# Kernel optimization log

Measured on AMD Instinct MI355X. Metric: run time of the kernel, lower is better.

The kernel has to match this reference:

```python
import jax, jax.numpy as jnp
import numpy as np
from jax import lax

STRIDES = (8, 16, 32, 64, 128)
LEVEL_HW = ((100, 128), (50, 64), (25, 32), (13, 16), (7, 8))
NUM_CLASSES = 80
PRE_NMS_THRESH = 0.05
PRE_NMS_TOPK = 1000
NMS_THRESH = 0.6
MAX_DET = 100
CLS_OFFSET = 1.0e4  # > max image coordinate, separates classes for joint NMS


def setup_inputs() -> dict:
    key = jax.random.key(0)
    B = 16
    ks = jax.random.split(key, 3 * len(LEVEL_HW))
    inp = {}
    i = 0
    for lvl, (h, w) in enumerate(LEVEL_HW):
        # shift logits down so sigmoid scores are mostly below the 0.05 candidate
        # threshold (realistic detection sparsity)
        inp[f"logits_p{lvl + 3}"] = jax.random.normal(ks[i], (B, NUM_CLASSES, h, w), jnp.float32) - 4.0; i += 1
        inp[f"bbox_p{lvl + 3}"] = jax.random.uniform(ks[i], (B, 4, h, w), jnp.float32, minval=0.0, maxval=64.0); i += 1
        inp[f"ctr_p{lvl + 3}"] = jax.random.normal(ks[i], (B, 1, h, w), jnp.float32); i += 1
    inp["im_info"] = jnp.tile(jnp.array([[800.0, 1024.0]], jnp.float32), (B, 1))
    return inp


def _locations(h, w, stride):
    # FCOSLocation: center of each stride cell -> [HW, 2] as (x, y)
    sx = jnp.arange(w, dtype=jnp.float32) * stride + stride // 2
    sy = jnp.arange(h, dtype=jnp.float32) * stride + stride // 2
    yy, xx = jnp.meshgrid(sy, sx, indexing="ij")
    return jnp.stack([xx.reshape(-1), yy.reshape(-1)], axis=-1)


def _nms_single(boxes, scores, classes):
    # boxes [K,4], scores [K] (descending), classes [K] int
    off = classes.astype(jnp.float32)[:, None] * CLS_OFFSET
    nb = boxes + off  # class-offset trick -> per-class NMS in one pass
    areas = jnp.maximum(nb[:, 2] - nb[:, 0], 0.0) * jnp.maximum(nb[:, 3] - nb[:, 1], 0.0)

    def body(sc, _):
        i = jnp.argmax(sc)
        s = sc[i]
        bi = nb[i]
        xx1 = jnp.maximum(bi[0], nb[:, 0])
        yy1 = jnp.maximum(bi[1], nb[:, 1])
        xx2 = jnp.minimum(bi[2], nb[:, 2])
        yy2 = jnp.minimum(bi[3], nb[:, 3])
        inter = jnp.maximum(xx2 - xx1, 0.0) * jnp.maximum(yy2 - yy1, 0.0)
        iou = inter / (areas[i] + areas - inter + 1e-9)
        sc2 = jnp.where(iou >= NMS_THRESH, -jnp.inf, sc).at[i].set(-jnp.inf)
        return sc2, (i, s > 0.0)

    _, (idxs, valid) = lax.scan(body, scores, None, length=MAX_DET)
    det = jnp.concatenate(
        [boxes[idxs], scores[idxs][:, None], classes[idxs].astype(jnp.float32)[:, None]],
        axis=-1,
    )  # [MAX_DET, 6] = x1,y1,x2,y2,score,class
    return jnp.where(valid[:, None], det, 0.0)


def _forward(logits_p3, bbox_p3, ctr_p3, logits_p4, bbox_p4, ctr_p4,
             logits_p5, bbox_p5, ctr_p5, logits_p6, bbox_p6, ctr_p6,
             logits_p7, bbox_p7, ctr_p7, im_info):
    levels = [(logits_p3, bbox_p3, ctr_p3), (logits_p4, bbox_p4, ctr_p4),
              (logits_p5, bbox_p5, ctr_p5), (logits_p6, bbox_p6, ctr_p6),
              (logits_p7, bbox_p7, ctr_p7)]
    scores_l, boxes_l = [], []
    for (lg, rg, ct), stride in zip(levels, STRIDES):
        B, C, H, W = lg.shape
        cls = jax.nn.sigmoid(lg).transpose(0, 2, 3, 1).reshape(B, H * W, C)
        cen = jax.nn.sigmoid(ct).transpose(0, 2, 3, 1).reshape(B, H * W, 1)
        # candidate threshold on raw class prob, then modulate by centerness
        comb = jnp.where(cls > PRE_NMS_THRESH, cls * cen, 0.0)
        locs = _locations(H, W, stride)  # [HW, 2]
        reg = rg.transpose(0, 2, 3, 1).reshape(B, H * W, 4)  # (l, t, r, b)
        bx = jnp.stack([locs[None, :, 0] - reg[..., 0],
                        locs[None, :, 1] - reg[..., 1],
                        locs[None, :, 0] + reg[..., 2],
                        locs[None, :, 1] + reg[..., 3]], axis=-1)
        scores_l.append(comb)
        boxes_l.append(bx)
    scores = jnp.concatenate(scores_l, axis=1)  # [B, N, C]
    boxes = jnp.concatenate(boxes_l, axis=1)    # [B, N, 4]
    B, N, C = scores.shape
    vals, idx = lax.top_k(scores.reshape(B, N * C), PRE_NMS_TOPK)  # [B, K]
    loc = idx // C
    cls_id = idx % C
    cand = jnp.take_along_axis(boxes, loc[..., None], axis=1)  # [B, K, 4]
    h = im_info[:, 0:1]
    w = im_info[:, 1:2]
    x1 = jnp.clip(cand[..., 0], 0.0, w - 1.0)
    y1 = jnp.clip(cand[..., 1], 0.0, h - 1.0)
    x2 = jnp.clip(cand[..., 2], 0.0, w - 1.0)
    y2 = jnp.clip(cand[..., 3], 0.0, h - 1.0)
    cand = jnp.stack([x1, y1, x2, y2], axis=-1)
    sc = jnp.where(vals > 0.0, jnp.sqrt(jnp.maximum(vals, 0.0) + 1e-12), 0.0)
    return jax.vmap(_nms_single)(cand, sc, cls_id)  # [B, MAX_DET, 6]


def reference(logits_p3, bbox_p3, ctr_p3, logits_p4, bbox_p4, ctr_p4,
              logits_p5, bbox_p5, ctr_p5, logits_p6, bbox_p6, ctr_p6,
              logits_p7, bbox_p7, ctr_p7, im_info):
    return _forward(logits_p3, bbox_p3, ctr_p3, logits_p4, bbox_p4, ctr_p4,
                    logits_p5, bbox_p5, ctr_p5, logits_p6, bbox_p6, ctr_p6,
                    logits_p7, bbox_p7, ctr_p7, im_info)
```

## Files before the change

kernel.cpp:

```cpp
#include <hip/hip_runtime.h>
#include <math.h>

#pragma clang fp contract(off)

#define NB 16
#define NC 80
#define NTOT 17064
#define TOPK 1000
#define NBINS 8192
#define CAP 4096
#define MAXDET 100
#define CNTSTRIDE 64
#define CHUNK 128
#define GH 128

struct Ptrs {
    const float* lg[5];
    const float* bb[5];
    const float* ct[5];
};

__device__ __forceinline__ void level_of(int n, int& l, int& hw, int& W,
                                         int& stride, int& half, int& HW) {
    if (n < 12800)      { l = 0; hw = n;         W = 128; stride = 8;   half = 4;  HW = 12800; }
    else if (n < 16000) { l = 1; hw = n - 12800; W = 64;  stride = 16;  half = 8;  HW = 3200;  }
    else if (n < 16800) { l = 2; hw = n - 16000; W = 32;  stride = 32;  half = 16; HW = 800;   }
    else if (n < 17008) { l = 3; hw = n - 16800; W = 16;  stride = 64;  half = 32; HW = 208;   }
    else                { l = 4; hw = n - 17008; W = 8;   stride = 128; half = 64; HW = 56;    }
}

__device__ __forceinline__ float fast_sig(float x) {
    float e = __expf(-x);
    return __builtin_amdgcn_rcpf(1.0f + e);
}

#define HG_ELEM(X, CT)                                                        \
    if ((X) > -2.47f) {                             \
        float cls = fast_sig(X);                                              \
        float cen = fast_sig(CT);                                             \
        unsigned bits = __float_as_uint(cls * cen);                           \
        if (bits >= FB_LO) {                                                  \
            int lb = (int)((bits - 32u) >> 19) - BINBASE;                     \
            lb = (lb < 0) ? 0 : ((lb > 63) ? 63 : lb);                        \
            atomicAdd(&whv[lb], 1u);                                          \
        }                                                                     \
    }

template<int HW4, int NF4>
__device__ __forceinline__ void histg_level(const float* lgb, const float* ctb,
        int tid, int bx, int gx, unsigned FB_LO, int BINBASE, unsigned* whv) {
    for (int i0 = bx * 512; i0 < NF4; i0 += gx * 512) {
        int ia = i0 + tid, ib = i0 + 256 + tid;
        bool la = ia < NF4, lb2 = ib < NF4;
        float4 va = make_float4(-9.f, -9.f, -9.f, -9.f);
        float4 vb = make_float4(-9.f, -9.f, -9.f, -9.f);
        int hwa = 0, hwb = 0;
        if (la) {
            int c = ia / HW4; hwa = ia - c * HW4;
            va = *(const float4*)(lgb + c * (HW4 * 4) + hwa * 4);
        }
        if (lb2) {
            int c = ib / HW4; hwb = ib - c * HW4;
            vb = *(const float4*)(lgb + c * (HW4 * 4) + hwb * 4);
        }
        if (va.x > -2.47f || va.y > -2.47f || va.z > -2.47f || va.w > -2.47f) {
            float4 cv = *(const float4*)(ctb + hwa * 4);
            HG_ELEM(va.x, cv.x) HG_ELEM(va.y, cv.y)
            HG_ELEM(va.z, cv.z) HG_ELEM(va.w, cv.w)
        }
        if (vb.x > -2.47f || vb.y > -2.47f || vb.z > -2.47f || vb.w > -2.47f) {
            float4 cv = *(const float4*)(ctb + hwb * 4);
            HG_ELEM(vb.x, cv.x) HG_ELEM(vb.y, cv.y)
            HG_ELEM(vb.z, cv.z) HG_ELEM(vb.w, cv.w)
        }
    }
}
#undef HG_ELEM

__global__ void __launch_bounds__(256) k_histB(Ptrs p, unsigned* hist, unsigned* cnt2) {
    __shared__ unsigned wh[4][64];
    int b = blockIdx.y, tid = threadIdx.x, bx = blockIdx.x, gx = gridDim.x;
    int wv = tid >> 6;
    if (bx == 0 && tid == 0) cnt2[(size_t)b * CNTSTRIDE] = 0;
    ((unsigned*)wh)[tid] = 0;
    __syncthreads();
    unsigned FB_LO = __float_as_uint(0.08f) - 64u;
    int BINBASE = (int)(__float_as_uint(0.08f) >> 19);
    unsigned* whv = wh[wv];

    histg_level<3200, 256000>(p.lg[0] + (size_t)b * NC * 12800, p.ct[0] + (size_t)b * 12800, tid, bx, gx, FB_LO, BINBASE, whv);
    histg_level< 800,  64000>(p.lg[1] + (size_t)b * NC * 3200,  p.ct[1] + (size_t)b * 3200,  tid, bx, gx, FB_LO, BINBASE, whv);
    histg_level< 200,  16000>(p.lg[2] + (size_t)b * NC * 800,   p.ct[2] + (size_t)b * 800,   tid, bx, gx, FB_LO, BINBASE, whv);
    histg_level<  52,   4160>(p.lg[3] + (size_t)b * NC * 208,   p.ct[3] + (size_t)b * 208,   tid, bx, gx, FB_LO, BINBASE, whv);
    histg_level<  14,   1120>(p.lg[4] + (size_t)b * NC * 56,    p.ct[4] + (size_t)b * 56,    tid, bx, gx, FB_LO, BINBASE, whv);

    __syncthreads();
    if (tid < 64) {
        unsigned s = wh[0][tid] + wh[1][tid] + wh[2][tid] + wh[3][tid];
        hist[((size_t)b * GH + bx) * 64 + tid] = s;
    }
}

template<int HW4, int NF4>
__device__ __forceinline__ void histf_level(const float* lgb, const float* ctb,
                                            int tid, unsigned* hist) {
    for (int i0 = 0; i0 < NF4; i0 += 256) {
        int i = i0 + tid;
        if (i < NF4) {
            int c = i / HW4, hwf = i - c * HW4;
            float4 v = *(const float4*)(lgb + c * (HW4 * 4) + hwf * 4);
            if (v.x > -2.95f || v.y > -2.95f || v.z > -2.95f || v.w > -2.95f) {
                float4 cv = *(const float4*)(ctb + hwf * 4);
                float xs[4] = {v.x, v.y, v.z, v.w};
                float cs[4] = {cv.x, cv.y, cv.z, cv.w};
#pragma unroll
                for (int j = 0; j < 4; ++j) {
                    float x = xs[j];
                    if (x > -2.95f) {
                        float cls = fast_sig(x);
                        if (cls > 0.04999f) {
                            bool in = true;
                            if (cls < 0.05001f)
                                in = (1.0f / (1.0f + expf(-x))) > 0.05f;
                            if (in) {
                                float cen = fast_sig(cs[j]);
                                unsigned bits = __float_as_uint(cls * cen);
                                unsigned cb = (bits > 32u) ? bits - 32u : 0u;
                                atomicAdd(&hist[cb >> 19], 1u);
                            }
                        }
                    }
                }
            }
        }
    }
}

__global__ void __launch_bounds__(256) k_thresh(Ptrs p, const unsigned* hist,
                                                unsigned* T) {
    __shared__ unsigned part[4][64];
    __shared__ unsigned red[64];
    __shared__ unsigned fullh[NBINS];
    __shared__ int s_T, s_ok;
    int b = blockIdx.x, tid = threadIdx.x;
    int bin = tid & 63, grp = tid >> 6;
    int BINBASE = (int)(__float_as_uint(0.08f) >> 19);

    unsigned s = 0;
    for (int blk = grp; blk < GH; blk += 4)
        s += hist[((size_t)b * GH + blk) * 64 + bin];
    part[grp][bin] = s;
    __syncthreads();
    if (tid < 64) red[tid] = part[0][tid] + part[1][tid] + part[2][tid] + part[3][tid];
    __syncthreads();
    if (tid == 0) {
        unsigned suf1 = 0;
        for (int i = 1; i < 64; ++i) suf1 += red[i];
        unsigned run = 0; int Tl = 0;
        for (int i = 63; i >= 1; --i) {
            run += red[i];
            if (run >= TOPK) { Tl = i; break; }
        }
        s_ok = (suf1 >= TOPK);
        s_T = Tl + BINBASE;
    }
    __syncthreads();

    if (!s_ok) {
        for (int i = tid; i < NBINS; i += 256) fullh[i] = 0;
        __syncthreads();
        histf_level<3200, 256000>(p.lg[0] + (size_t)b * NC * 12800, p.ct[0] + (size_t)b * 12800, tid, fullh);
        histf_level< 800,  64000>(p.lg[1] + (size_t)b * NC * 3200,  p.ct[1] + (size_t)b * 3200,  tid, fullh);
        histf_level< 200,  16000>(p.lg[2] + (size_t)b * NC * 800,   p.ct[2] + (size_t)b * 800,   tid, fullh);
        histf_level<  52,   4160>(p.lg[3] + (size_t)b * NC * 208,   p.ct[3] + (size_t)b * 208,   tid, fullh);
        histf_level<  14,   1120>(p.lg[4] + (size_t)b * NC * 56,    p.ct[4] + (size_t)b * 56,    tid, fullh);
        __syncthreads();
        if (tid == 0) {
            unsigned run = 0; int Tf = 0;
            for (int i = NBINS - 1; i >= 0; --i) {
                run += fullh[i];
                if (run >= TOPK) { Tf = i; break; }
            }
            s_T = Tf;
        }
        __syncthreads();
    }
    if (tid == 0) T[b] = (unsigned)s_T;
}

#define CD_J(J, X, CT, NB0, CC, F, K)                                         \
    if ((X) > xpre) {                                                         \
        float cls = 1.0f / (1.0f + expf(-(X)));                               \
        if (cls > 0.05f) {                                                    \
            float cen = 1.0f / (1.0f + expf(-(CT)));                          \
            float comb = cls * cen;                                           \
            unsigned bits = __float_as_uint(comb);                            \
            if ((bits >> 19) >= Tb) {                                         \
                unsigned idx = (unsigned)(((NB0) + (J)) * NC + (CC));         \
                K = ((unsigned long long)bits << 32) | (0xFFFFFFFFu - idx);   \
                F = true;                                                     \
            }                                                                 \
        }                                                                     \
    }

template<int HW4, int NF4, int LVOFF>
__device__ __forceinline__ void compact_level(const float* lgb, const float* ctb,
        int tid, int lane, int bx, int gx, unsigned Tb, float xpre,
        unsigned* cntb, unsigned long long* selb, unsigned long long ltmask) {
    for (int i0 = bx * 512; i0 < NF4; i0 += gx * 512) {
        int ia = i0 + tid, ib2 = i0 + 256 + tid;
        bool la = ia < NF4, lb2 = ib2 < NF4;
        float4 va = make_float4(-9.f, -9.f, -9.f, -9.f);
        float4 vb = make_float4(-9.f, -9.f, -9.f, -9.f);
        int hwa = 0, hwb = 0, cca = 0, ccb = 0;
        if (la) {
            cca = ia / HW4; hwa = ia - cca * HW4;
            va = *(const float4*)(lgb + cca * (HW4 * 4) + hwa * 4);
        }
        if (lb2) {
            ccb = ib2 / HW4; hwb = ib2 - ccb * HW4;
            vb = *(const float4*)(lgb + ccb * (HW4 * 4) + hwb * 4);
        }
        {
            bool f0 = false, f1 = false, f2 = false, f3 = false;
            unsigned long long k0 = 0, k1 = 0, k2 = 0, k3 = 0;
            if (va.x > xpre || va.y > xpre || va.z > xpre || va.w > xpre) {
                float4 cv = *(const float4*)(ctb + hwa * 4);
                int nb0 = LVOFF + hwa * 4;
                CD_J(0, va.x, cv.x, nb0, cca, f0, k0)
                CD_J(1, va.y, cv.y, nb0, cca, f1, k1)
                CD_J(2, va.z, cv.z, nb0, cca, f2, k2)
                CD_J(3, va.w, cv.w, nb0, cca, f3, k3)
            }
            unsigned long long m0 = __ballot(f0), m1 = __ballot(f1);
            unsigned long long m2 = __ballot(f2), m3 = __ballot(f3);
            if (m0 | m1 | m2 | m3) {
                unsigned t0 = (unsigned)__popcll(m0), t1 = (unsigned)__popcll(m1);
                unsigned t2 = (unsigned)__popcll(m2), t3 = (unsigned)__popcll(m3);
                int basep = 0;
                if (lane == 0) basep = (int)atomicAdd(cntb, t0 + t1 + t2 + t3);
                basep = __shfl(basep, 0);
                if (f0) { int pos = basep + (int)__popcll(m0 & ltmask);                       if (pos < CAP) selb[pos] = k0; }
                if (f1) { int pos = basep + (int)t0 + (int)__popcll(m1 & ltmask);             if (pos < CAP) selb[pos] = k1; }
                if (f2) { int pos = basep + (int)(t0 + t1) + (int)__popcll(m2 & ltmask);      if (pos < CAP) selb[pos] = k2; }
                if (f3) { int pos = basep + (int)(t0 + t1 + t2) + (int)__popcll(m3 & ltmask); if (pos < CAP) selb[pos] = k3; }
            }
        }
        {
            bool f0 = false, f1 = false, f2 = false, f3 = false;
            unsigned long long k0 = 0, k1 = 0, k2 = 0, k3 = 0;
            if (vb.x > xpre || vb.y > xpre || vb.z > xpre || vb.w > xpre) {
                float4 cv = *(const float4*)(ctb + hwb * 4);
                int nb0 = LVOFF + hwb * 4;
                CD_J(0, vb.x, cv.x, nb0, ccb, f0, k0)
                CD_J(1, vb.y, cv.y, nb0, ccb, f1, k1)
                CD_J(2, vb.z, cv.z, nb0, ccb, f2, k2)
                CD_J(3, vb.w, cv.w, nb0, ccb, f3, k3)
            }
            unsigned long long m0 = __ballot(f0), m1 = __ballot(f1);
            unsigned long long m2 = __ballot(f2), m3 = __ballot(f3);
            if (m0 | m1 | m2 | m3) {
                unsigned t0 = (unsigned)__popcll(m0), t1 = (unsigned)__popcll(m1);
                unsigned t2 = (unsigned)__popcll(m2), t3 = (unsigned)__popcll(m3);
                int basep = 0;
                if (lane == 0) basep = (int)atomicAdd(cntb, t0 + t1 + t2 + t3);
                basep = __shfl(basep, 0);
                if (f0) { int pos = basep + (int)__popcll(m0 & ltmask);                       if (pos < CAP) selb[pos] = k0; }
                if (f1) { int pos = basep + (int)t0 + (int)__popcll(m1 & ltmask);             if (pos < CAP) selb[pos] = k1; }
                if (f2) { int pos = basep + (int)(t0 + t1) + (int)__popcll(m2 & ltmask);      if (pos < CAP) selb[pos] = k2; }
                if (f3) { int pos = basep + (int)(t0 + t1 + t2) + (int)__popcll(m3 & ltmask); if (pos < CAP) selb[pos] = k3; }
            }
        }
    }
}
#undef CD_J

__global__ void __launch_bounds__(256) k_compactB(Ptrs p, const unsigned* T,
                                                  unsigned* cnt2, unsigned long long* sel) {
    int b = blockIdx.y, tid = threadIdx.x, lane = tid & 63;
    int bx = blockIdx.x, gx = gridDim.x;
    unsigned Tb = T[b];
    float mthr = __uint_as_float(Tb << 19);
    float xpre = -2.95f;
    if (mthr > 1e-37f && mthr < 1.0f) {
        float lm = logf(mthr / (1.0f - mthr)) - 0.01f;
        if (lm > xpre) xpre = lm;
    }
    unsigned long long ltmask = (1ULL << lane) - 1ULL;
    unsigned* cntb = cnt2 + (size_t)b * CNTSTRIDE;
    unsigned long long* selb = sel + (size_t)b * CAP;
    compact_level<3200, 256000,     0>(p.lg[0] + (size_t)b * NC * 12800, p.ct[0] + (size_t)b * 12800, tid, lane, bx, gx, Tb, xpre, cntb, selb, ltmask);
    compact_level< 800,  64000, 12800>(p.lg[1] + (size_t)b * NC * 3200,  p.ct[1] + (size_t)b * 3200,  tid, lane, bx, gx, Tb, xpre, cntb, selb, ltmask);
    compact_level< 200,  16000, 16000>(p.lg[2] + (size_t)b * NC * 800,   p.ct[2] + (size_t)b * 800,   tid, lane, bx, gx, Tb, xpre, cntb, selb, ltmask);
    compact_level<  52,   4160, 16800>(p.lg[3] + (size_t)b * NC * 208,   p.ct[3] + (size_t)b * 208,   tid, lane, bx, gx, Tb, xpre, cntb, selb, ltmask);
    compact_level<  14,   1120, 17008>(p.lg[4] + (size_t)b * NC * 56,    p.ct[4] + (size_t)b * 56,    tid, lane, bx, gx, Tb, xpre, cntb, selb, ltmask);
}

__global__ void __launch_bounds__(256) k_rankdec(Ptrs p, const unsigned* cnt,
                                                 const unsigned long long* sel,
                                                 const float* im_info, float* cand) {
    __shared__ __align__(16) unsigned long long keys[CAP];
    int b = blockIdx.y, tid = threadIdx.x;
    unsigned M = cnt[(size_t)b * CNTSTRIDE];
    if (M > CAP) M = CAP;
    int s0 = blockIdx.x * 256;
    if (s0 >= (int)M) return;
    int Mpad = (int)((M + 1u) & ~1u);
    for (int i = tid; i < Mpad; i += 256)
        keys[i] = (i < (int)M) ? sel[(size_t)b * CAP + i] : 0ULL;
    __syncthreads();

    int s = s0 + tid;
    if (s >= (int)M) return;
    unsigned long long k = keys[s];
    int rank = 0;
    for (int j = 0; j < Mpad; j += 2) {
        ulonglong2 kk = *(const ulonglong2*)&keys[j];
        rank += (kk.x > k) ? 1 : 0;
        rank += (kk.y > k) ? 1 : 0;
    }
    if (rank >= TOPK) return;

    float Him = im_info[b * 2 + 0], Wim = im_info[b * 2 + 1];
    float xmax = Wim - 1.0f, ymax = Him - 1.0f;
    unsigned sb = (unsigned)(k >> 32);
    unsigned idx = 0xFFFFFFFFu - (unsigned)(k & 0xFFFFFFFFu);
    float val = __uint_as_float(sb);
    int n = idx / NC, c = idx - n * NC;
    int l, hw, W, stride, half, HW;
    level_of(n, l, hw, W, stride, half, HW);
    int wx = hw % W, hy = hw / W;
    float locx = (float)(wx * stride + half);
    float locy = (float)(hy * stride + half);
    const float* bb = p.bb[l] + (size_t)b * 4 * HW + hw;
    float r0 = bb[0], r1 = bb[(size_t)HW], r2 = bb[(size_t)2 * HW], r3 = bb[(size_t)3 * HW];
    float x1 = locx - r0, y1 = locy - r1, x2 = locx + r2, y2 = locy + r3;
    x1 = fminf(fmaxf(x1, 0.f), xmax);
    y1 = fminf(fmaxf(y1, 0.f), ymax);
    x2 = fminf(fmaxf(x2, 0.f), xmax);
    y2 = fminf(fmaxf(y2, 0.f), ymax);
    float scv = sqrtf(val + 1e-12f);
    float off = (float)c * 10000.0f;
    float a0 = x1 + off, a1 = y1 + off, a2 = x2 + off, a3 = y2 + off;
    float area = fmaxf(a2 - a0, 0.f) * fmaxf(a3 - a1, 0.f);
    float* dst = cand + ((size_t)b * TOPK + rank) * 12;
    *(float4*)(dst + 0) = make_float4(x1, y1, x2, y2);
    *(float4*)(dst + 4) = make_float4(a0, a1, a2, a3);
    *(float4*)(dst + 8) = make_float4(area, scv, (float)c, 0.f);
}

__global__ void __launch_bounds__(64) k_nms(const unsigned* cnt, const float* cand,
                                            float* out) {
    __shared__ float4 s_ob[CHUNK], s_nb[CHUNK], s_ms[CHUNK];
    int b = blockIdx.x, lane = threadIdx.x;
    unsigned M = cnt[(size_t)b * CNTSTRIDE];
    if (M > CAP) M = CAP;
    int ncand = (int)M < TOPK ? (int)M : TOPK;
    const float* src = cand + (size_t)b * TOPK * 12;
    float* ob = out + (size_t)b * MAXDET * 6;

    int na = 0;
    float4 a0b = make_float4(0.f, 0.f, 0.f, 0.f);
    float4 a1b = make_float4(0.f, 0.f, 0.f, 0.f);
    float a0a = 0.f, a1a = 0.f;

    for (int base = 0; base < ncand && na < MAXDET; base += CHUNK) {
        int cn = ncand - base; if (cn > CHUNK) cn = CHUNK;
        for (int cidx = lane; cidx < cn; cidx += 64) {
            const float* s = src + (size_t)(base + cidx) * 12;
            s_ob[cidx] = *(const float4*)(s + 0);
            s_nb[cidx] = *(const float4*)(s + 4);
            s_ms[cidx] = *(const float4*)(s + 8);
        }
        __syncthreads();
        for (int r = 0; r < cn && na < MAXDET; ++r) {
            float4 cb = s_nb[r];
            float ca = s_ms[r].x;
            bool sup = false;
            if (lane < na) {
                float xx1 = fmaxf(a0b.x, cb.x);
                float yy1 = fmaxf(a0b.y, cb.y);
                float xx2 = fminf(a0b.z, cb.z);
                float yy2 = fminf(a0b.w, cb.w);
                float inter = fmaxf(xx2 - xx1, 0.f) * fmaxf(yy2 - yy1, 0.f);
                float iou = inter / (((a0a + ca) - inter) + 1e-9f);
                sup = (iou >= 0.6f);
            }
            if (lane + 64 < na) {
                float xx1 = fmaxf(a1b.x, cb.x);
                float yy1 = fmaxf(a1b.y, cb.y);
                float xx2 = fminf(a1b.z, cb.z);
                float yy2 = fminf(a1b.w, cb.w);
                float inter = fmaxf(xx2 - xx1, 0.f) * fmaxf(yy2 - yy1, 0.f);
                float iou = inter / (((a1a + ca) - inter) + 1e-9f);
                sup |= (iou >= 0.6f);
            }
            if (__ballot(sup) == 0ULL) {
                if (lane == (na & 63)) {
                    if (na < 64) { a0b = cb; a0a = ca; }
                    else         { a1b = cb; a1a = ca; }
                }
                if (lane == 0) {
                    float4 o4 = s_ob[r]; float4 m4 = s_ms[r];
                    ob[na * 6 + 0] = o4.x; ob[na * 6 + 1] = o4.y;
                    ob[na * 6 + 2] = o4.z; ob[na * 6 + 3] = o4.w;
                    ob[na * 6 + 4] = m4.y; ob[na * 6 + 5] = m4.z;
                }
                ++na;
            }
        }
        __syncthreads();
    }
    for (int q = na * 6 + lane; q < MAXDET * 6; q += 64)
        ob[q] = 0.f;
}

extern "C" void kernel_launch(void* const* d_in, const int* in_sizes, int n_in,
                              void* d_out, int out_size, void* d_ws, size_t ws_size,
                              hipStream_t stream) {
    Ptrs p;
    for (int l = 0; l < 5; ++l) {
        p.lg[l] = (const float*)d_in[3 * l + 0];
        p.bb[l] = (const float*)d_in[3 * l + 1];
        p.ct[l] = (const float*)d_in[3 * l + 2];
    }
    const float* im_info = (const float*)d_in[15];
    float* out = (float*)d_out;
    unsigned char* w = (unsigned char*)d_ws;

    unsigned* hist          = (unsigned*)(w);
    unsigned* cnt2          = (unsigned*)(w + 524288);
    unsigned* T             = (unsigned*)(w + 528384);
    unsigned long long* sel = (unsigned long long*)(w + 528640);
    float* cand             = (float*)(w + 1052928);

    k_histB<<<dim3(GH, NB), 256, 0, stream>>>(p, hist, cnt2);
    k_thresh<<<NB, 256, 0, stream>>>(p, hist, T);
    k_compactB<<<dim3(GH, NB), 256, 0, stream>>>(p, T, cnt2, sel);
    k_rankdec<<<dim3(16, NB), 256, 0, stream>>>(p, cnt2, sel, im_info, cand);
    k_nms<<<NB, 64, 0, stream>>>(cnt2, cand, out);
}
```

Before: 237.8 us.

## Record candidate keys during histogram pass and filter them instead of rescanning logits

The histogram kernel now also appends every above-floor candidate (score bits and flat index) to a per-block segment buffer in workspace. A merged threshold+filter kernel then computes the threshold per image and, when no segment overflowed, compacts only those recorded candidates by re-deriving exact scores from gathered logits. This avoids a second full pass over all logits and removes one launch. It falls back to a full rescan on overflow or when the coarse histogram is insufficient, and it adds shared-memory atomics to the hot histogram loop and a larger workspace.

```diff
diff --git a/kernel.cpp b/kernel.cpp
--- a/kernel.cpp
+++ b/kernel.cpp
@@ -13,6 +13,8 @@
 #define CNTSTRIDE 64
 #define CHUNK 128
 #define GH 128
+#define SEGCAP 768
+#define FB 16
 
 struct Ptrs {
     const float* lg[5];
@@ -34,7 +36,7 @@
     return __builtin_amdgcn_rcpf(1.0f + e);
 }
 
-#define HG_ELEM(X, CT)                                                        \
+#define HG_ELEM(X, CT, J, CC, NB0)                                            \
     if ((X) > -2.47f) {                             \
         float cls = fast_sig(X);                                              \
         float cen = fast_sig(CT);                                             \
@@ -43,62 +45,75 @@
             int lb = (int)((bits - 32u) >> 19) - BINBASE;                     \
             lb = (lb < 0) ? 0 : ((lb > 63) ? 63 : lb);                        \
             atomicAdd(&whv[lb], 1u);                                          \
+            unsigned pos = atomicAdd(s_na, 1u);                               \
+            if (pos < SEGCAP) {                                               \
+                unsigned idx = (unsigned)(((NB0) + (J)) * NC + (CC));         \
+                segb[pos] = ((unsigned long long)bits << 32) | idx;           \
+            }                                                                 \
         }                                                                     \
     }
 
-template<int HW4, int NF4>
+template<int HW4, int NF4, int LVOFF>
 __device__ __forceinline__ void histg_level(const float* lgb, const float* ctb,
-        int tid, int bx, int gx, unsigned FB_LO, int BINBASE, unsigned* whv) {
+        int tid, int bx, int gx, unsigned FB_LO, int BINBASE, unsigned* whv,
+        unsigned* s_na, unsigned long long* segb) {
     for (int i0 = bx * 512; i0 < NF4; i0 += gx * 512) {
         int ia = i0 + tid, ib = i0 + 256 + tid;
         bool la = ia < NF4, lb2 = ib < NF4;
         float4 va = make_float4(-9.f, -9.f, -9.f, -9.f);
         float4 vb = make_float4(-9.f, -9.f, -9.f, -9.f);
-        int hwa = 0, hwb = 0;
+        int hwa = 0, hwb = 0, cca = 0, ccb = 0;
         if (la) {
-            int c = ia / HW4; hwa = ia - c * HW4;
-            va = *(const float4*)(lgb + c * (HW4 * 4) + hwa * 4);
+            cca = ia / HW4; hwa = ia - cca * HW4;
+            va = *(const float4*)(lgb + cca * (HW4 * 4) + hwa * 4);
         }
         if (lb2) {
-            int c = ib / HW4; hwb = ib - c * HW4;
-            vb = *(const float4*)(lgb + c * (HW4 * 4) + hwb * 4);
+            ccb = ib / HW4; hwb = ib - ccb * HW4;
+            vb = *(const float4*)(lgb + ccb * (HW4 * 4) + hwb * 4);
         }
         if (va.x > -2.47f || va.y > -2.47f || va.z > -2.47f || va.w > -2.47f) {
             float4 cv = *(const float4*)(ctb + hwa * 4);
-            HG_ELEM(va.x, cv.x) HG_ELEM(va.y, cv.y)
-            HG_ELEM(va.z, cv.z) HG_ELEM(va.w, cv.w)
+            int nb0 = LVOFF + hwa * 4;
+            HG_ELEM(va.x, cv.x, 0, cca, nb0) HG_ELEM(va.y, cv.y, 1, cca, nb0)
+            HG_ELEM(va.z, cv.z, 2, cca, nb0) HG_ELEM(va.w, cv.w, 3, cca, nb0)
         }
         if (vb.x > -2.47f || vb.y > -2.47f || vb.z > -2.47f || vb.w > -2.47f) {
             float4 cv = *(const float4*)(ctb + hwb * 4);
-            HG_ELEM(vb.x, cv.x) HG_ELEM(vb.y, cv.y)
-            HG_ELEM(vb.z, cv.z) HG_ELEM(vb.w, cv.w)
+            int nb0 = LVOFF + hwb * 4;
+            HG_ELEM(vb.x, cv.x, 0, ccb, nb0) HG_ELEM(vb.y, cv.y, 1, ccb, nb0)
+            HG_ELEM(vb.z, cv.z, 2, ccb, nb0) HG_ELEM(vb.w, cv.w, 3, ccb, nb0)
         }
     }
 }
 #undef HG_ELEM
 
-__global__ void __launch_bounds__(256) k_histB(Ptrs p, unsigned* hist, unsigned* cnt2) {
+__global__ void __launch_bounds__(256) k_histB(Ptrs p, unsigned* hist, unsigned* cnt2,
+                                               unsigned* blkcnt, unsigned long long* segs) {
     __shared__ unsigned wh[4][64];
+    __shared__ unsigned s_na;
     int b = blockIdx.y, tid = threadIdx.x, bx = blockIdx.x, gx = gridDim.x;
     int wv = tid >> 6;
     if (bx == 0 && tid == 0) cnt2[(size_t)b * CNTSTRIDE] = 0;
     ((unsigned*)wh)[tid] = 0;
+    if (tid == 0) s_na = 0;
     __syncthreads();
     unsigned FB_LO = __float_as_uint(0.08f) - 64u;
     int BINBASE = (int)(__float_as_uint(0.08f) >> 19);
     unsigned* whv = wh[wv];
-
-    histg_level<3200, 256000>(p.lg[0] + (size_t)b * NC * 12800, p.ct[0] + (size_t)b * 12800, tid, bx, gx, FB_LO, BINBASE, whv);
-    histg_level< 800,  64000>(p.lg[1] + (size_t)b * NC * 3200,  p.ct[1] + (size_t)b * 3200,  tid, bx, gx, FB_LO, BINBASE, whv);
-    histg_level< 200,  16000>(p.lg[2] + (size_t)b * NC * 800,   p.ct[2] + (size_t)b * 800,   tid, bx, gx, FB_LO, BINBASE, whv);
-    histg_level<  52,   4160>(p.lg[3] + (size_t)b * NC * 208,   p.ct[3] + (size_t)b * 208,   tid, bx, gx, FB_LO, BINBASE, whv);
-    histg_level<  14,   1120>(p.lg[4] + (size_t)b * NC * 56,    p.ct[4] + (size_t)b * 56,    tid, bx, gx, FB_LO, BINBASE, whv);
+    unsigned long long* segb = segs + ((size_t)b * GH + bx) * SEGCAP;
+
+    histg_level<3200, 256000,     0>(p.lg[0] + (size_t)b * NC * 12800, p.ct[0] + (size_t)b * 12800, tid, bx, gx, FB_LO, BINBASE, whv, &s_na, segb);
+    histg_level< 800,  64000, 12800>(p.lg[1] + (size_t)b * NC * 3200,  p.ct[1] + (size_t)b * 3200,  tid, bx, gx, FB_LO, BINBASE, whv, &s_na, segb);
+    histg_level< 200,  16000, 16000>(p.lg[2] + (size_t)b * NC * 800,   p.ct[2] + (size_t)b * 800,   tid, bx, gx, FB_LO, BINBASE, whv, &s_na, segb);
+    histg_level<  52,   4160, 16800>(p.lg[3] + (size_t)b * NC * 208,   p.ct[3] + (size_t)b * 208,   tid, bx, gx, FB_LO, BINBASE, whv, &s_na, segb);
+    histg_level<  14,   1120, 17008>(p.lg[4] + (size_t)b * NC * 56,    p.ct[4] + (size_t)b * 56,    tid, bx, gx, FB_LO, BINBASE, whv, &s_na, segb);
 
     __syncthreads();
     if (tid < 64) {
         unsigned s = wh[0][tid] + wh[1][tid] + wh[2][tid] + wh[3][tid];
         hist[((size_t)b * GH + bx) * 64 + tid] = s;
     }
+    if (tid == 0) blkcnt[(size_t)b * GH + bx] = s_na;
 }
 
 template<int HW4, int NF4>
@@ -136,22 +151,134 @@
     }
 }
 
-__global__ void __launch_bounds__(256) k_thresh(Ptrs p, const unsigned* hist,
-                                                unsigned* T) {
+#define CD_J(J, X, CT, NB0, CC, F, K)                                         \
+    if ((X) > xpre) {                                                         \
+        float cls = 1.0f / (1.0f + expf(-(X)));                               \
+        if (cls > 0.05f) {                                                    \
+            float cen = 1.0f / (1.0f + expf(-(CT)));                          \
+            float comb = cls * cen;                                           \
+            unsigned bits = __float_as_uint(comb);                            \
+            if ((bits >> 19) >= Tb) {                                         \
+                unsigned idx = (unsigned)(((NB0) + (J)) * NC + (CC));         \
+                K = ((unsigned long long)bits << 32) | (0xFFFFFFFFu - idx);   \
+                F = true;                                                     \
+            }                                                                 \
+        }                                                                     \
+    }
+
+template<int HW4, int NF4, int LVOFF>
+__device__ __forceinline__ void compact_level(const float* lgb, const float* ctb,
+        int tid, int lane, int bx, int gx, unsigned Tb, float xpre,
+        unsigned* cntb, unsigned long long* selb, unsigned long long ltmask) {
+    for (int i0 = bx * 512; i0 < NF4; i0 += gx * 512) {
+        int ia = i0 + tid, ib2 = i0 + 256 + tid;
+        bool la = ia < NF4, lb2 = ib2 < NF4;
+        float4 va = make_float4(-9.f, -9.f, -9.f, -9.f);
+        float4 vb = make_float4(-9.f, -9.f, -9.f, -9.f);
+        int hwa = 0, hwb = 0, cca = 0, ccb = 0;
+        if (la) {
+            cca = ia / HW4; hwa = ia - cca * HW4;
+            va = *(const float4*)(lgb + cca * (HW4 * 4) + hwa * 4);
+        }
+        if (lb2) {
+            ccb = ib2 / HW4; hwb = ib2 - ccb * HW4;
+            vb = *(const float4*)(lgb + ccb * (HW4 * 4) + hwb * 4);
+        }
+        {
+            bool f0 = false, f1 = false, f2 = false, f3 = false;
+            unsigned long long k0 = 0, k1 = 0, k2 = 0, k3 = 0;
+            if (va.x > xpre || va.y > xpre || va.z > xpre || va.w > xpre) {
+                float4 cv = *(const float4*)(ctb + hwa * 4);
+                int nb0 = LVOFF + hwa * 4;
+                CD_J(0, va.x, cv.x, nb0, cca, f0, k0)
+                CD_J(1, va.y, cv.y, nb0, cca, f1, k1)
+                CD_J(2, va.z, cv.z, nb0, cca, f2, k2)
+                CD_J(3, va.w, cv.w, nb0, cca, f3, k3)
+            }
+            unsigned long long m0 = __ballot(f0), m1 = __ballot(f1);
+            unsigned long long m2 = __ballot(f2), m3 = __ballot(f3);
+            if (m0 | m1 | m2 | m3) {
+                unsigned t0 = (unsigned)__popcll(m0), t1 = (unsigned)__popcll(m1);
+                unsigned t2 = (unsigned)__popcll(m2), t3 = (unsigned)__popcll(m3);
+                int basep = 0;
+                if (lane == 0) basep = (int)atomicAdd(cntb, t0 + t1 + t2 + t3);
+                basep = __shfl(basep, 0);
+                if (f0) { int pos = basep + (int)__popcll(m0 & ltmask);                       if (pos < CAP) selb[pos] = k0; }
+                if (f1) { int pos = basep + (int)t0 + (int)__popcll(m1 & ltmask);             if (pos < CAP) selb[pos] = k1; }
+                if (f2) { int pos = basep + (int)(t0 + t1) + (int)__popcll(m2 & ltmask);      if (pos < CAP) selb[pos] = k2; }
+                if (f3) { int pos = basep + (int)(t0 + t1 + t2) + (int)__popcll(m3 & ltmask); if (pos < CAP) selb[pos] = k3; }
+            }
+        }
+        {
+            bool f0 = false, f1 = false, f2 = false, f3 = false;
+            unsigned long long k0 = 0, k1 = 0, k2 = 0, k3 = 0;
+            if (vb.x > xpre || vb.y > xpre || vb.z > xpre || vb.w > xpre) {
+                float4 cv = *(const float4*)(ctb + hwb * 4);
+                int nb0 = LVOFF + hwb * 4;
+                CD_J(0, vb.x, cv.x, nb0, ccb, f0, k0)
+                CD_J(1, vb.y, cv.y, nb0, ccb, f1, k1)
+                CD_J(2, vb.z, cv.z, nb0, ccb, f2, k2)
+                CD_J(3, vb.w, cv.w, nb0, ccb, f3, k3)
+            }
+            unsigned long long m0 = __ballot(f0), m1 = __ballot(f1);
+            unsigned long long m2 = __ballot(f2), m3 = __ballot(f3);
+            if (m0 | m1 | m2 | m3) {
+                unsigned t0 = (unsigned)__popcll(m0), t1 = (unsigned)__popcll(m1);
+                unsigned t2 = (unsigned)__popcll(m2), t3 = (unsigned)__popcll(m3);
+                int basep = 0;
+                if (lane == 0) basep = (int)atomicAdd(cntb, t0 + t1 + t2 + t3);
+                basep = __shfl(basep, 0);
+                if (f0) { int pos = basep + (int)__popcll(m0 & ltmask);                       if (pos < CAP) selb[pos] = k0; }
+                if (f1) { int pos = basep + (int)t0 + (int)__popcll(m1 & ltmask);             if (pos < CAP) selb[pos] = k1; }
+                if (f2) { int pos = basep + (int)(t0 + t1) + (int)__popcll(m2 & ltmask);      if (pos < CAP) selb[pos] = k2; }
+                if (f3) { int pos = basep + (int)(t0 + t1 + t2) + (int)__popcll(m3 & ltmask); if (pos < CAP) selb[pos] = k3; }
+            }
+        }
+    }
+}
+#undef CD_J
+
+__device__ __forceinline__ void run_compact(const Ptrs& p, int b, int tid, int lane,
+        int bx, int gx, unsigned Tb, unsigned* cnt2, unsigned long long* sel) {
+    float mthr = __uint_as_float(Tb << 19);
+    float xpre = -2.95f;
+    if (mthr > 1e-37f && mthr < 1.0f) {
+        float lm = logf(mthr / (1.0f - mthr)) - 0.01f;
+        if (lm > xpre) xpre = lm;
+    }
+    unsigned long long ltmask = (1ULL << lane) - 1ULL;
+    unsigned* cntb = cnt2 + (size_t)b * CNTSTRIDE;
+    unsigned long long* selb = sel + (size_t)b * CAP;
+    compact_level<3200, 256000,     0>(p.lg[0] + (size_t)b * NC * 12800, p.ct[0] + (size_t)b * 12800, tid, lane, bx, gx, Tb, xpre, cntb, selb, ltmask);
+    compact_level< 800,  64000, 12800>(p.lg[1] + (size_t)b * NC * 3200,  p.ct[1] + (size_t)b * 3200,  tid, lane, bx, gx, Tb, xpre, cntb, selb, ltmask);
+    compact_level< 200,  16000, 16000>(p.lg[2] + (size_t)b * NC * 800,   p.ct[2] + (size_t)b * 800,   tid, lane, bx, gx, Tb, xpre, cntb, selb, ltmask);
+    compact_level<  52,   4160, 16800>(p.lg[3] + (size_t)b * NC * 208,   p.ct[3] + (size_t)b * 208,   tid, lane, bx, gx, Tb, xpre, cntb, selb, ltmask);
+    compact_level<  14,   1120, 17008>(p.lg[4] + (size_t)b * NC * 56,    p.ct[4] + (size_t)b * 56,    tid, lane, bx, gx, Tb, xpre, cntb, selb, ltmask);
+}
+
+__global__ void __launch_bounds__(256) k_filter(Ptrs p, const unsigned* hist,
+        const unsigned* blkcnt, const unsigned long long* segs,
+        unsigned* cnt2, unsigned long long* sel) {
     __shared__ unsigned part[4][64];
     __shared__ unsigned red[64];
     __shared__ unsigned fullh[NBINS];
     __shared__ int s_T, s_ok;
-    int b = blockIdx.x, tid = threadIdx.x;
-    int bin = tid & 63, grp = tid >> 6;
+    __shared__ unsigned s_ovf;
+    int b = blockIdx.y, tid = threadIdx.x, bx = blockIdx.x;
+    int bin = tid & 63, grp = tid >> 6, lane = tid & 63;
     int BINBASE = (int)(__float_as_uint(0.08f) >> 19);
 
     unsigned s = 0;
     for (int blk = grp; blk < GH; blk += 4)
         s += hist[((size_t)b * GH + blk) * 64 + bin];
     part[grp][bin] = s;
+    if (tid == 0) s_ovf = 0;
     __syncthreads();
     if (tid < 64) red[tid] = part[0][tid] + part[1][tid] + part[2][tid] + part[3][tid];
+    unsigned ov = 0;
+    for (int i = tid; i < GH; i += 256)
+        ov |= (blkcnt[(size_t)b * GH + i] > SEGCAP) ? 1u : 0u;
+    if (ov) atomicOr(&s_ovf, 1u);
     __syncthreads();
     if (tid == 0) {
         unsigned suf1 = 0;
@@ -166,7 +293,58 @@
     }
     __syncthreads();
 
+    if (s_ok && !s_ovf) {
+        unsigned Tb = (unsigned)s_T;
+        unsigned FLO = (Tb << 19) - 64u;
+        unsigned* cntb = cnt2 + (size_t)b * CNTSTRIDE;
+        unsigned long long* selb = sel + (size_t)b * CAP;
+        unsigned long long ltmask = (1ULL << lane) - 1ULL;
+        for (int sg = bx; sg < GH; sg += FB) {
+            unsigned cs = blkcnt[(size_t)b * GH + sg];
+            if (cs > SEGCAP) cs = SEGCAP;
+            const unsigned long long* sp = segs + ((size_t)b * GH + sg) * SEGCAP;
+            for (unsigned e0 = 0; e0 < cs; e0 += 256) {
+                unsigned e = e0 + (unsigned)tid;
+                bool take = false;
+                unsigned long long key = 0;
+                if (e < cs) {
+                    unsigned long long kk = sp[e];
+                    if ((unsigned)(kk >> 32) >= FLO) {
+                        unsigned idx = (unsigned)kk;
+                        int n = (int)(idx / NC), c = (int)(idx - (unsigned)n * NC);
+                        int l, hw, W, stride, half, HW;
+                        level_of(n, l, hw, W, stride, half, HW);
+                        float x   = p.lg[l][(size_t)b * NC * HW + (size_t)c * HW + hw];
+                        float ctv = p.ct[l][(size_t)b * HW + hw];
+                        float cls = 1.0f / (1.0f + expf(-x));
+                        if (cls > 0.05f) {
+                            float cen = 1.0f / (1.0f + expf(-ctv));
+                            unsigned bits = __float_as_uint(cls * cen);
+                            if ((bits >> 19) >= Tb) {
+                                key = ((unsigned long long)bits << 32) | (0xFFFFFFFFu - idx);
+                                take = true;
+                            }
+                        }
+                    }
+                }
+                unsigned long long m = __ballot(take);
+                if (m) {
+                    unsigned tot = (unsigned)__popcll(m);
+                    int basep = 0;
+                    if (lane == 0) basep = (int)atomicAdd(cntb, tot);
+                    basep = __shfl(basep, 0);
+                    if (take) {
+                        int pos = basep + (int)__popcll(m & ltmask);
+                        if (pos < CAP) selb[pos] = key;
+                    }
+                }
+            }
+        }
+        return;
+    }
+
     if (!s_ok) {
+        if (bx != 0) return;
         for (int i = tid; i < NBINS; i += 256) fullh[i] = 0;
         __syncthreads();
         histf_level<3200, 256000>(p.lg[0] + (size_t)b * NC * 12800, p.ct[0] + (size_t)b * 12800, tid, fullh);
@@ -184,116 +362,11 @@
             s_T = Tf;
         }
         __syncthreads();
-    }
-    if (tid == 0) T[b] = (unsigned)s_T;
-}
-
-#define CD_J(J, X, CT, NB0, CC, F, K)                                         \
-    if ((X) > xpre) {                                                         \
-        float cls = 1.0f / (1.0f + expf(-(X)));                               \
-        if (cls > 0.05f) {                                                    \
-            float cen = 1.0f / (1.0f + expf(-(CT)));                          \
-            float comb = cls * cen;                                           \
-            unsigned bits = __float_as_uint(comb);                            \
-            if ((bits >> 19) >= Tb) {                                         \
-                unsigned idx = (unsigned)(((NB0) + (J)) * NC + (CC));         \
-                K = ((unsigned long long)bits << 32) | (0xFFFFFFFFu - idx);   \
-                F = true;                                                     \
-            }                                                                 \
-        }                                                                     \
-    }
-
-template<int HW4, int NF4, int LVOFF>
-__device__ __forceinline__ void compact_level(const float* lgb, const float* ctb,
-        int tid, int lane, int bx, int gx, unsigned Tb, float xpre,
-        unsigned* cntb, unsigned long long* selb, unsigned long long ltmask) {
-    for (int i0 = bx * 512; i0 < NF4; i0 += gx * 512) {
-        int ia = i0 + tid, ib2 = i0 + 256 + tid;
-        bool la = ia < NF4, lb2 = ib2 < NF4;
-        float4 va = make_float4(-9.f, -9.f, -9.f, -9.f);
-        float4 vb = make_float4(-9.f, -9.f, -9.f, -9.f);
-        int hwa = 0, hwb = 0, cca = 0, ccb = 0;
-        if (la) {
-            cca = ia / HW4; hwa = ia - cca * HW4;
-            va = *(const float4*)(lgb + cca * (HW4 * 4) + hwa * 4);
-        }
-        if (lb2) {
-            ccb = ib2 / HW4; hwb = ib2 - ccb * HW4;
-            vb = *(const float4*)(lgb + ccb * (HW4 * 4) + hwb * 4);
-        }
-        {
-            bool f0 = false, f1 = false, f2 = false, f3 = false;
-            unsigned long long k0 = 0, k1 = 0, k2 = 0, k3 = 0;
-            if (va.x > xpre || va.y > xpre || va.z > xpre || va.w > xpre) {
-                float4 cv = *(const float4*)(ctb + hwa * 4);
-                int nb0 = LVOFF + hwa * 4;
-                CD_J(0, va.x, cv.x, nb0, cca, f0, k0)
-                CD_J(1, va.y, cv.y, nb0, cca, f1, k1)
-                CD_J(2, va.z, cv.z, nb0, cca, f2, k2)
-                CD_J(3, va.w, cv.w, nb0, cca, f3, k3)
-            }
-            unsigned long long m0 = __ballot(f0), m1 = __ballot(f1);
-            unsigned long long m2 = __ballot(f2), m3 = __ballot(f3);
-            if (m0 | m1 | m2 | m3) {
-                unsigned t0 = (unsigned)__popcll(m0), t1 = (unsigned)__popcll(m1);
-                unsigned t2 = (unsigned)__popcll(m2), t3 = (unsigned)__popcll(m3);
-                int basep = 0;
-                if (lane == 0) basep = (int)atomicAdd(cntb, t0 + t1 + t2 + t3);
-                basep = __shfl(basep, 0);
-                if (f0) { int pos = basep + (int)__popcll(m0 & ltmask);                       if (pos < CAP) selb[pos] = k0; }
-                if (f1) { int pos = basep + (int)t0 + (int)__popcll(m1 & ltmask);             if (pos < CAP) selb[pos] = k1; }
-                if (f2) { int pos = basep + (int)(t0 + t1) + (int)__popcll(m2 & ltmask);      if (pos < CAP) selb[pos] = k2; }
-                if (f3) { int pos = basep + (int)(t0 + t1 + t2) + (int)__popcll(m3 & ltmask); if (pos < CAP) selb[pos] = k3; }
-            }
-        }
-        {
-            bool f0 = false, f1 = false, f2 = false, f3 = false;
-            unsigned long long k0 = 0, k1 = 0, k2 = 0, k3 = 0;
-            if (vb.x > xpre || vb.y > xpre || vb.z > xpre || vb.w > xpre) {
-                float4 cv = *(const float4*)(ctb + hwb * 4);
-                int nb0 = LVOFF + hwb * 4;
-                CD_J(0, vb.x, cv.x, nb0, ccb, f0, k0)
-                CD_J(1, vb.y, cv.y, nb0, ccb, f1, k1)
-                CD_J(2, vb.z, cv.z, nb0, ccb, f2, k2)
-                CD_J(3, vb.w, cv.w, nb0, ccb, f3, k3)
-            }
-            unsigned long long m0 = __ballot(f0), m1 = __ballot(f1);
-            unsigned long long m2 = __ballot(f2), m3 = __ballot(f3);
-            if (m0 | m1 | m2 | m3) {
-                unsigned t0 = (unsigned)__popcll(m0), t1 = (unsigned)__popcll(m1);
-                unsigned t2 = (unsigned)__popcll(m2), t3 = (unsigned)__popcll(m3);
-                int basep = 0;
-                if (lane == 0) basep = (int)atomicAdd(cntb, t0 + t1 + t2 + t3);
-                basep = __shfl(basep, 0);
-                if (f0) { int pos = basep + (int)__popcll(m0 & ltmask);                       if (pos < CAP) selb[pos] = k0; }
-                if (f1) { int pos = basep + (int)t0 + (int)__popcll(m1 & ltmask);             if (pos < CAP) selb[pos] = k1; }
-                if (f2) { int pos = basep + (int)(t0 + t1) + (int)__popcll(m2 & ltmask);      if (pos < CAP) selb[pos] = k2; }
-                if (f3) { int pos = basep + (int)(t0 + t1 + t2) + (int)__popcll(m3 & ltmask); if (pos < CAP) selb[pos] = k3; }
-            }
-        }
-    }
-}
-#undef CD_J
-
-__global__ void __launch_bounds__(256) k_compactB(Ptrs p, const unsigned* T,
-                                                  unsigned* cnt2, unsigned long long* sel) {
-    int b = blockIdx.y, tid = threadIdx.x, lane = tid & 63;
-    int bx = blockIdx.x, gx = gridDim.x;
-    unsigned Tb = T[b];
-    float mthr = __uint_as_float(Tb << 19);
-    float xpre = -2.95f;
-    if (mthr > 1e-37f && mthr < 1.0f) {
-        float lm = logf(mthr / (1.0f - mthr)) - 0.01f;
-        if (lm > xpre) xpre = lm;
-    }
-    unsigned long long ltmask = (1ULL << lane) - 1ULL;
-    unsigned* cntb = cnt2 + (size_t)b * CNTSTRIDE;
-    unsigned long long* selb = sel + (size_t)b * CAP;
-    compact_level<3200, 256000,     0>(p.lg[0] + (size_t)b * NC * 12800, p.ct[0] + (size_t)b * 12800, tid, lane, bx, gx, Tb, xpre, cntb, selb, ltmask);
-    compact_level< 800,  64000, 12800>(p.lg[1] + (size_t)b * NC * 3200,  p.ct[1] + (size_t)b * 3200,  tid, lane, bx, gx, Tb, xpre, cntb, selb, ltmask);
-    compact_level< 200,  16000, 16000>(p.lg[2] + (size_t)b * NC * 800,   p.ct[2] + (size_t)b * 800,   tid, lane, bx, gx, Tb, xpre, cntb, selb, ltmask);
-    compact_level<  52,   4160, 16800>(p.lg[3] + (size_t)b * NC * 208,   p.ct[3] + (size_t)b * 208,   tid, lane, bx, gx, Tb, xpre, cntb, selb, ltmask);
-    compact_level<  14,   1120, 17008>(p.lg[4] + (size_t)b * NC * 56,    p.ct[4] + (size_t)b * 56,    tid, lane, bx, gx, Tb, xpre, cntb, selb, ltmask);
+        run_compact(p, b, tid, lane, 0, 1, (unsigned)s_T, cnt2, sel);
+        return;
+    }
+
+    run_compact(p, b, tid, lane, bx, FB, (unsigned)s_T, cnt2, sel);
 }
 
 __global__ void __launch_bounds__(256) k_rankdec(Ptrs p, const unsigned* cnt,
@@ -430,13 +503,13 @@
 
     unsigned* hist          = (unsigned*)(w);
     unsigned* cnt2          = (unsigned*)(w + 524288);
-    unsigned* T             = (unsigned*)(w + 528384);
-    unsigned long long* sel = (unsigned long long*)(w + 528640);
-    float* cand             = (float*)(w + 1052928);
-
-    k_histB<<<dim3(GH, NB), 256, 0, stream>>>(p, hist, cnt2);
-    k_thresh<<<NB, 256, 0, stream>>>(p, hist, T);
-    k_compactB<<<dim3(GH, NB), 256, 0, stream>>>(p, T, cnt2, sel);
+    unsigned* blkcnt        = (unsigned*)(w + 528384);
+    unsigned long long* segs = (unsigned long long*)(w + 536576);
+    unsigned long long* sel = (unsigned long long*)(w + 13119488);
+    float* cand             = (float*)(w + 13643776);
+
+    k_histB<<<dim3(GH, NB), 256, 0, stream>>>(p, hist, cnt2, blkcnt, segs);
+    k_filter<<<dim3(FB, NB), 256, 0, stream>>>(p, hist, blkcnt, segs, cnt2, sel);
     k_rankdec<<<dim3(16, NB), 256, 0, stream>>>(p, cnt2, sel, im_info, cand);
     k_nms<<<NB, 64, 0, stream>>>(cnt2, cand, out);
 }
```

After: 241.4 us. Within noise of the previous version (+1.5%).
